# Kernel tuning notes

Hardware: AMD Instinct MI355X
Metric: run time of the kernel (lower is better)

The kernel has to match this reference:

```python
import jax, jax.numpy as jnp
import numpy as np

N_NODES = 50000
N_EDGES = 800000
D_NODE = 64
D_ATTR = 16
D_T = 16
D_OUT = 128


def setup_inputs() -> dict:
    key = jax.random.key(0)
    ks = jax.random.split(key, 8)
    x = jax.random.normal(ks[0], (N_NODES, D_NODE), dtype=jnp.float32)
    edge_index = jax.random.randint(ks[1], (2, N_EDGES), 0, N_NODES, dtype=jnp.int64)
    edge_attr = jax.random.normal(ks[2], (N_EDGES, D_ATTR), dtype=jnp.float32)
    edge_t = jax.random.normal(ks[3], (N_EDGES, D_T), dtype=jnp.float32)
    d_msg = D_NODE + D_ATTR + D_T  # 96, = in_channels[0]
    Wm = jax.random.normal(ks[4], (d_msg, D_OUT), dtype=jnp.float32) / np.sqrt(d_msg)
    bm = jnp.zeros((D_OUT,), dtype=jnp.float32)
    Wr = jax.random.normal(ks[5], (D_NODE, D_OUT), dtype=jnp.float32) / np.sqrt(D_NODE)
    br = jnp.zeros((D_OUT,), dtype=jnp.float32)
    return {"x": x, "edge_index": edge_index, "edge_attr": edge_attr,
            "edge_t": edge_t, "Wm": Wm, "bm": bm, "Wr": Wr, "br": br}


def reference(x, edge_index, edge_attr, edge_t, Wm, bm, Wr, br):
    row, col = edge_index[0], edge_index[1]
    # gather source node feats and concat edge features -> [E, 96]
    msg = jnp.concatenate([x[col], edge_attr, edge_t], axis=1)
    # scatter-sum messages to destination nodes -> [N, 96]
    agg = jax.ops.segment_sum(msg, row, num_segments=x.shape[0])
    x_j = agg @ Wm + bm          # lin_m
    x_i = x @ Wr + br            # lin_r
    out = 0.5 * x_j + x_i        # normalize=False path
    return out
```

## Files before the change

### kernel.cpp

```cpp
#include <hip/hip_runtime.h>
#include <hip/hip_bf16.h>

#define NN 50000
#define NE 800000
#define D_NODE 64
#define D_MSG 96
#define D_K 160
#define D_OUT 128
#define KP 168

#define SCAN_BLOCKS 49

typedef __attribute__((ext_vector_type(8))) short bf16x8;
typedef __attribute__((ext_vector_type(4))) float f32x4;

#define CNT_OFF  0
#define OFF_OFF  200000
#define CUR_OFF  400000
#define PERM_OFF 600000
#define A_OFF    7000064
#define BSUM_OFF 23000064
#define WS_NEEDED (BSUM_OFF + SCAN_BLOCKS * 4)

__device__ __forceinline__ unsigned short f2bf(float f) {
    __hip_bfloat16 h = __float2bfloat16(f);
    union { __hip_bfloat16 h; unsigned short u; } c; c.h = h;
    return c.u;
}

__global__ __launch_bounds__(256) void hist_kernel(
    const int* __restrict__ row, int* __restrict__ cnt)
{
    int e = blockIdx.x * blockDim.x + threadIdx.x;
    if (e < NE) atomicAdd(&cnt[row[e]], 1);
}

__global__ __launch_bounds__(256) void scanA_kernel(
    const int* __restrict__ cnt, int* __restrict__ bsum)
{
    const int t = threadIdx.x, b = blockIdx.x;
    const int idx4 = b * 256 + t;
    int s = 0;
    if (idx4 < NN / 4) {
        int4 c = ((const int4*)cnt)[idx4];
        s = c.x + c.y + c.z + c.w;
    }
    for (int d = 32; d > 0; d >>= 1) s += __shfl_down(s, d);
    __shared__ int wsum[4];
    if ((t & 63) == 0) wsum[t >> 6] = s;
    __syncthreads();
    if (t == 0) bsum[b] = wsum[0] + wsum[1] + wsum[2] + wsum[3];
}

__global__ __launch_bounds__(64) void scanB_kernel(int* __restrict__ bsum)
{
    const int t = threadIdx.x;
    int v = (t < SCAN_BLOCKS) ? bsum[t] : 0;
    int orig = v;
    for (int d = 1; d < 64; d <<= 1) {
        int u = __shfl_up(v, d);
        if (t >= d) v += u;
    }
    if (t < SCAN_BLOCKS) bsum[t] = v - orig;
}

__global__ __launch_bounds__(256) void scanC_kernel(
    const int* __restrict__ cnt, const int* __restrict__ bsum,
    int* __restrict__ off, int* __restrict__ cur)
{
    const int t = threadIdx.x, b = blockIdx.x;
    const int idx4 = b * 256 + t;
    const bool valid = (idx4 < NN / 4);
    int4 c = make_int4(0, 0, 0, 0);
    if (valid) c = ((const int4*)cnt)[idx4];
    int s = c.x + c.y + c.z + c.w;

    const int lane = t & 63, w = t >> 6;
    int v = s;
    for (int d = 1; d < 64; d <<= 1) {
        int u = __shfl_up(v, d);
        if (lane >= d) v += u;
    }
    __shared__ int wsum[4];
    if (lane == 63) wsum[w] = v;
    __syncthreads();
    int woff = 0;
    for (int i = 0; i < 4; ++i) if (i < w) woff += wsum[i];

    if (valid) {
        int excl = (v - s) + woff + bsum[b];
        int4 o;
        o.x = excl;
        o.y = o.x + c.x;
        o.z = o.y + c.y;
        o.w = o.z + c.z;
        ((int4*)off)[idx4] = o;
        ((int4*)cur)[idx4] = o;
    }
}

__global__ __launch_bounds__(256) void bucket_kernel(
    const int* __restrict__ row, const int* __restrict__ col,
    int* __restrict__ cur, int2* __restrict__ perm)
{
    int e = blockIdx.x * blockDim.x + threadIdx.x;
    if (e >= NE) return;
    int pos = atomicAdd(&cur[row[e]], 1);
    perm[pos] = make_int2(e, col[e]);
}

__global__ __launch_bounds__(256) void gather_kernel(
    const float* __restrict__ x,
    const float* __restrict__ ea,
    const float* __restrict__ et,
    const int*  __restrict__ off,
    const int*  __restrict__ cnt,
    const int2* __restrict__ perm,
    unsigned short* __restrict__ A)
{
    const int node = blockIdx.x * 4 + (threadIdx.x >> 6);
    const int lane = threadIdx.x & 63;
    if (node >= NN) return;

    const int beg = off[node];
    const int n   = cnt[node];

    const float* eb = (lane < 16) ? (ea + lane) : (et + (lane - 16));

    float a0 = 0.f, a1 = 0.f, a2 = 0.f, a3 = 0.f;
    float b0 = 0.f, b1 = 0.f, b2 = 0.f, b3 = 0.f;
    int j = 0;
    for (; j + 4 <= n; j += 4) {
        int2 p0 = perm[beg + j];
        int2 p1 = perm[beg + j + 1];
        int2 p2 = perm[beg + j + 2];
        int2 p3 = perm[beg + j + 3];
        a0 += x[(size_t)p0.y * D_NODE + lane];
        a1 += x[(size_t)p1.y * D_NODE + lane];
        a2 += x[(size_t)p2.y * D_NODE + lane];
        a3 += x[(size_t)p3.y * D_NODE + lane];
        if (lane < 32) {
            b0 += eb[(size_t)p0.x * 16];
            b1 += eb[(size_t)p1.x * 16];
            b2 += eb[(size_t)p2.x * 16];
            b3 += eb[(size_t)p3.x * 16];
        }
    }
    for (; j < n; ++j) {
        int2 p = perm[beg + j];
        a0 += x[(size_t)p.y * D_NODE + lane];
        if (lane < 32) b0 += eb[(size_t)p.x * 16];
    }
    float accx = (a0 + a1) + (a2 + a3);
    float acce = (b0 + b1) + (b2 + b3);

    unsigned short* dst = A + (size_t)node * D_K;
    dst[lane] = f2bf(0.5f * accx);
    if (lane < 32) dst[D_NODE + lane] = f2bf(0.5f * acce);
    dst[D_MSG + lane] = f2bf(x[(size_t)node * D_NODE + lane]);
}

__global__ __launch_bounds__(256) void mfma_dense_kernel(
    const unsigned short* __restrict__ A,
    const float* __restrict__ Wm,
    const float* __restrict__ bm,
    const float* __restrict__ Wr,
    const float* __restrict__ br,
    float*       __restrict__ out)
{
    __shared__ unsigned short Bt[D_OUT * KP];

    for (int i = threadIdx.x; i < D_K * D_OUT; i += 256) {
        int k = i >> 7, n = i & 127;
        float v = (k < D_MSG) ? Wm[i] : Wr[i - D_MSG * D_OUT];
        Bt[n * KP + k] = f2bf(v);
    }
    __syncthreads();

    const int l   = threadIdx.x & 63;
    const int wid = threadIdx.x >> 6;
    const int wm  = wid & 1;
    const int wn  = wid >> 1;
    const int lr  = l & 15;
    const int lk  = (l >> 4) << 3;

    bf16x8 bq[4][5];
#pragma unroll
    for (int nf = 0; nf < 4; ++nf) {
        int c = wn * 64 + nf * 16 + lr;
#pragma unroll
        for (int ks = 0; ks < 5; ++ks)
            bq[nf][ks] = *(const bf16x8*)(&Bt[c * KP + ks * 32 + lk]);
    }

    const int row0 = blockIdx.x * 64 + wm * 32;

    f32x4 acc[2][4];
#pragma unroll
    for (int mf = 0; mf < 2; ++mf)
#pragma unroll
        for (int nf = 0; nf < 4; ++nf)
            acc[mf][nf] = (f32x4){0.f, 0.f, 0.f, 0.f};

#pragma unroll
    for (int ks = 0; ks < 5; ++ks) {
#pragma unroll
        for (int mf = 0; mf < 2; ++mf) {
            int row = row0 + mf * 16 + lr;
            if (row > NN - 1) row = NN - 1;
            bf16x8 af = *(const bf16x8*)(A + (size_t)row * D_K + ks * 32 + lk);
#pragma unroll
            for (int nf = 0; nf < 4; ++nf)
                acc[mf][nf] = __builtin_amdgcn_mfma_f32_16x16x32_bf16(
                    af, bq[nf][ks], acc[mf][nf], 0, 0, 0);
        }
    }

#pragma unroll
    for (int nf = 0; nf < 4; ++nf) {
        int c = wn * 64 + nf * 16 + lr;
        float bias = 0.5f * bm[c] + br[c];
#pragma unroll
        for (int mf = 0; mf < 2; ++mf) {
            int rbase = row0 + mf * 16 + ((l >> 4) << 2);
#pragma unroll
            for (int r = 0; r < 4; ++r) {
                int row = rbase + r;
                if (row < NN) out[(size_t)row * D_OUT + c] = acc[mf][nf][r] + bias;
            }
        }
    }
}

extern "C" void kernel_launch(void* const* d_in, const int* in_sizes, int n_in,
                              void* d_out, int out_size, void* d_ws, size_t ws_size,
                              hipStream_t stream) {
    const float* x  = (const float*)d_in[0];
    const int*   ei = (const int*)d_in[1];
    const float* ea = (const float*)d_in[2];
    const float* et = (const float*)d_in[3];
    const float* Wm = (const float*)d_in[4];
    const float* bm = (const float*)d_in[5];
    const float* Wr = (const float*)d_in[6];
    const float* br = (const float*)d_in[7];
    float* out = (float*)d_out;
    const int* row = ei;
    const int* col = ei + NE;

    char* ws = (char*)d_ws;
    int*  cnt  = (int*)(ws + CNT_OFF);
    int*  off  = (int*)(ws + OFF_OFF);
    int*  cur  = (int*)(ws + CUR_OFF);
    int2* perm = (int2*)(ws + PERM_OFF);
    int*  bsum = (int*)(ws + BSUM_OFF);
    unsigned short* A = (unsigned short*)(ws + A_OFF);

    hipMemsetAsync(cnt, 0, NN * sizeof(int), stream);
    hist_kernel  <<<(NE + 255) / 256, 256, 0, stream>>>(row, cnt);
    scanA_kernel <<<SCAN_BLOCKS, 256, 0, stream>>>(cnt, bsum);
    scanB_kernel <<<1, 64, 0, stream>>>(bsum);
    scanC_kernel <<<SCAN_BLOCKS, 256, 0, stream>>>(cnt, bsum, off, cur);
    bucket_kernel<<<(NE + 255) / 256, 256, 0, stream>>>(row, col, cur, perm);
    gather_kernel<<<(NN + 3) / 4, 256, 0, stream>>>(x, ea, et, off, cnt, perm, A);
    mfma_dense_kernel<<<(NN + 63) / 64, 256, 0, stream>>>(A, Wm, bm, Wr, br, out);
}
```

Measured before the change: 183.2 us.

## Pre-cast x to bf16 and gather two edges per wave using half-wave split

A new kernel casts x to bf16 once, writing it into the self-feature columns of the A matrix. The gather kernel then reads neighbour features from that bf16 copy, halving gathered bytes. Each wave splits into two halves that take alternating edges: every lane loads two packed bf16 features per edge, and 32 lanes cover the attr and time columns. The halves are combined with a cross-half shuffle. This costs an extra launch and rounds the summed neighbour features to bf16 before accumulation, which loses some precision.

New measurement: 179.0 us. -2.3%, faster.

```diff
diff --git a/kernel.cpp b/kernel.cpp
--- a/kernel.cpp
+++ b/kernel.cpp
@@ -26,6 +26,22 @@
     __hip_bfloat16 h = __float2bfloat16(f);
     union { __hip_bfloat16 h; unsigned short u; } c; c.h = h;
     return c.u;
+}
+__device__ __forceinline__ float bf2f(unsigned int u) {
+    union { unsigned int i; float f; } c; c.i = u << 16; return c.f;
+}
+
+__global__ __launch_bounds__(256) void xcast_kernel(
+    const float* __restrict__ x, unsigned short* __restrict__ A)
+{
+    int t = blockIdx.x * 256 + threadIdx.x;
+    if (t >= NN * 16) return;
+    int node = t >> 4, c4 = t & 15;
+    float4 v = *(const float4*)(x + (size_t)node * D_NODE + c4 * 4);
+    uint2 pk;
+    pk.x = (unsigned)f2bf(v.x) | ((unsigned)f2bf(v.y) << 16);
+    pk.y = (unsigned)f2bf(v.z) | ((unsigned)f2bf(v.w) << 16);
+    *(uint2*)(A + (size_t)node * D_K + D_MSG + c4 * 4) = pk;
 }
 
 __global__ __launch_bounds__(256) void hist_kernel(
@@ -110,7 +126,6 @@
 }
 
 __global__ __launch_bounds__(256) void gather_kernel(
-    const float* __restrict__ x,
     const float* __restrict__ ea,
     const float* __restrict__ et,
     const int*  __restrict__ off,
@@ -123,41 +138,74 @@
     if (node >= NN) return;
 
     const int beg = off[node];
-    const int n   = cnt[node];
-
-    const float* eb = (lane < 16) ? (ea + lane) : (et + (lane - 16));
-
-    float a0 = 0.f, a1 = 0.f, a2 = 0.f, a3 = 0.f;
-    float b0 = 0.f, b1 = 0.f, b2 = 0.f, b3 = 0.f;
-    int j = 0;
-    for (; j + 4 <= n; j += 4) {
-        int2 p0 = perm[beg + j];
-        int2 p1 = perm[beg + j + 1];
-        int2 p2 = perm[beg + j + 2];
-        int2 p3 = perm[beg + j + 3];
-        a0 += x[(size_t)p0.y * D_NODE + lane];
-        a1 += x[(size_t)p1.y * D_NODE + lane];
-        a2 += x[(size_t)p2.y * D_NODE + lane];
-        a3 += x[(size_t)p3.y * D_NODE + lane];
-        if (lane < 32) {
-            b0 += eb[(size_t)p0.x * 16];
-            b1 += eb[(size_t)p1.x * 16];
-            b2 += eb[(size_t)p2.x * 16];
-            b3 += eb[(size_t)p3.x * 16];
+    const int end = beg + cnt[node];
+
+    const int half = lane >> 5;
+    const int hl   = lane & 31;
+    const float* ebase = ((lane >> 4) & 1) ? et : ea;
+    const int ecol = lane & 15;
+
+    float accx0 = 0.f, accx1 = 0.f;
+    float acce  = 0.f;
+
+    int j = beg;
+    if ((j & 1) && j < end) {
+        int2 p = perm[j];
+        if (half == 0) {
+            unsigned xv = *(const unsigned*)(A + (size_t)p.y * D_K + D_MSG + hl * 2);
+            accx0 += bf2f(xv & 0xffffu);
+            accx1 += bf2f(xv >> 16);
+            acce  += ebase[(size_t)p.x * 16 + ecol];
         }
-    }
-    for (; j < n; ++j) {
-        int2 p = perm[beg + j];
-        a0 += x[(size_t)p.y * D_NODE + lane];
-        if (lane < 32) b0 += eb[(size_t)p.x * 16];
-    }
-    float accx = (a0 + a1) + (a2 + a3);
-    float acce = (b0 + b1) + (b2 + b3);
+        ++j;
+    }
+    for (; j + 4 <= end; j += 4) {
+        int4 q0 = *(const int4*)(perm + j);
+        int4 q1 = *(const int4*)(perm + j + 2);
+        int c01 = half ? q0.w : q0.y;
+        int e01 = half ? q0.z : q0.x;
+        int c23 = half ? q1.w : q1.y;
+        int e23 = half ? q1.z : q1.x;
+        unsigned xv0 = *(const unsigned*)(A + (size_t)c01 * D_K + D_MSG + hl * 2);
+        unsigned xv1 = *(const unsigned*)(A + (size_t)c23 * D_K + D_MSG + hl * 2);
+        float ev0 = ebase[(size_t)e01 * 16 + ecol];
+        float ev1 = ebase[(size_t)e23 * 16 + ecol];
+        accx0 += bf2f(xv0 & 0xffffu) + bf2f(xv1 & 0xffffu);
+        accx1 += bf2f(xv0 >> 16)     + bf2f(xv1 >> 16);
+        acce  += ev0 + ev1;
+    }
+    if (j + 2 <= end) {
+        int4 q0 = *(const int4*)(perm + j);
+        int c01 = half ? q0.w : q0.y;
+        int e01 = half ? q0.z : q0.x;
+        unsigned xv0 = *(const unsigned*)(A + (size_t)c01 * D_K + D_MSG + hl * 2);
+        accx0 += bf2f(xv0 & 0xffffu);
+        accx1 += bf2f(xv0 >> 16);
+        acce  += ebase[(size_t)e01 * 16 + ecol];
+        j += 2;
+    }
+    if (j < end) {
+        int2 p = perm[j];
+        if (half == 0) {
+            unsigned xv = *(const unsigned*)(A + (size_t)p.y * D_K + D_MSG + hl * 2);
+            accx0 += bf2f(xv & 0xffffu);
+            accx1 += bf2f(xv >> 16);
+            acce  += ebase[(size_t)p.x * 16 + ecol];
+        }
+    }
+
+    accx0 += __shfl_xor(accx0, 32);
+    accx1 += __shfl_xor(accx1, 32);
+    acce  += __shfl_xor(acce, 32);
 
     unsigned short* dst = A + (size_t)node * D_K;
-    dst[lane] = f2bf(0.5f * accx);
-    if (lane < 32) dst[D_NODE + lane] = f2bf(0.5f * acce);
-    dst[D_MSG + lane] = f2bf(x[(size_t)node * D_NODE + lane]);
+    if (half == 0) {
+        unsigned pk = (unsigned)f2bf(0.5f * accx0)
+                    | ((unsigned)f2bf(0.5f * accx1) << 16);
+        *(unsigned*)(dst + hl * 2) = pk;
+    } else {
+        dst[D_NODE + hl] = f2bf(0.5f * acce);
+    }
 }
 
 __global__ __launch_bounds__(256) void mfma_dense_kernel(
@@ -256,11 +304,12 @@
     unsigned short* A = (unsigned short*)(ws + A_OFF);
 
     hipMemsetAsync(cnt, 0, NN * sizeof(int), stream);
+    xcast_kernel <<<(NN * 16 + 255) / 256, 256, 0, stream>>>(x, A);
     hist_kernel  <<<(NE + 255) / 256, 256, 0, stream>>>(row, cnt);
     scanA_kernel <<<SCAN_BLOCKS, 256, 0, stream>>>(cnt, bsum);
     scanB_kernel <<<1, 64, 0, stream>>>(bsum);
     scanC_kernel <<<SCAN_BLOCKS, 256, 0, stream>>>(cnt, bsum, off, cur);
     bucket_kernel<<<(NE + 255) / 256, 256, 0, stream>>>(row, col, cur, perm);
-    gather_kernel<<<(NN + 3) / 4, 256, 0, stream>>>(x, ea, et, off, cnt, perm, A);
+    gather_kernel<<<(NN + 3) / 4, 256, 0, stream>>>(ea, et, off, cnt, perm, A);
     mfma_dense_kernel<<<(NN + 63) / 64, 256, 0, stream>>>(A, Wm, bm, Wr, br, out);
 }
```
